# Performance work log

Measured on AMD Instinct MI355X. Metric: run time of the kernel, lower is better.

The kernel has to match this reference:

```python
import jax, jax.numpy as jnp
import numpy as np
import math

N = 8192
NFEAT = 63
NHID = 1024
NLAYERS = 7
LAMBDA = 1.5
ALPHA = 0.7
NEG = -1e12


def setup_inputs() -> dict:
    key = jax.random.key(0)
    ks = jax.random.split(key, 12)
    x = jax.random.normal(ks[0], (N, NFEAT), dtype=jnp.float32)
    # dist acts as a (normalized) propagation matrix; scale by 1/N for numerical stability
    dist = jax.random.uniform(ks[1], (N, N), dtype=jnp.float32) / N
    adj = jax.random.randint(ks[2], (N, N), 0, 2, dtype=jnp.int32)
    # parameters
    fc_W = jax.random.normal(ks[3], (NFEAT, NHID), dtype=jnp.float32) * 0.1
    fc_b = jnp.zeros((NHID,), dtype=jnp.float32)
    stdv = 1.0 / math.sqrt(NHID)
    conv_W = jax.random.uniform(ks[4], (NLAYERS, NHID, NHID), dtype=jnp.float32,
                                minval=-stdv, maxval=stdv)
    gat_W = jax.random.normal(ks[5], (NHID, NHID), dtype=jnp.float32) * (1.414 / math.sqrt(NHID))
    gat_a = jax.random.normal(ks[6], (2 * NHID, 1), dtype=jnp.float32) * 0.05
    cls1_W = jax.random.normal(ks[7], (NHID, 64), dtype=jnp.float32) * (1.0 / math.sqrt(NHID))
    cls1_b = jnp.zeros((64,), dtype=jnp.float32)
    cls3_W = jax.random.normal(ks[8], (64, 1), dtype=jnp.float32) * 0.125
    cls3_b = jnp.zeros((1,), dtype=jnp.float32)
    return {"x": x, "dist": dist, "adj": adj, "fc_W": fc_W, "fc_b": fc_b,
            "conv_W": conv_W, "gat_W": gat_W, "gat_a": gat_a,
            "cls1_W": cls1_W, "cls1_b": cls1_b, "cls3_W": cls3_W, "cls3_b": cls3_b}


def _theta(l):
    return min(1.0, math.log(LAMBDA / l + 1.0))


def reference(x, dist, adj, fc_W, fc_b, conv_W, gat_W, gat_a, cls1_W, cls1_b, cls3_W, cls3_b):
    # eval mode: all dropouts are identity
    h = jax.nn.relu(x @ fc_W + fc_b)          # [N, H]
    h0 = h
    # GCNII-style propagation layers
    for i in range(NLAYERS):
        theta = _theta(i + 1)
        hi = dist @ h                          # [N, H] sparse-style propagation
        support = (1.0 - ALPHA) * hi + ALPHA * h0
        out = theta * (support @ conv_W[i]) + (1.0 - theta) * support + h
        h = jax.nn.relu(out)
    # GAT layer (l = 9). Faithful math, but computed without the N*N*2F tensor:
    # e_ij = leakyrelu(h_i' @ a1 + h_j' @ a2) with h' = h @ W
    hp = h @ gat_W                             # [N, H]
    a1 = gat_a[:NHID, 0]                       # [H]
    a2 = gat_a[NHID:, 0]                       # [H]
    e = jax.nn.leaky_relu(hp @ a1[:, None] + (hp @ a2[:, None]).T, negative_slope=0.2)  # [N, N]
    e = jnp.where(adj > 0, e, NEG)
    attention = jax.nn.softmax(e, axis=1)      # [N, N]
    theta = _theta(9)
    hi = attention @ h                         # note: attends over layer input h, not hp
    support = (1.0 - ALPHA) * hi + ALPHA * h0
    out = theta * (support @ gat_W) + (1.0 - theta) * support + h
    h = jax.nn.elu(out)
    h = jax.nn.relu(h @ cls1_W + cls1_b)
    out = jax.nn.sigmoid(h @ cls3_W + cls3_b)  # [N, 1]
    return out.squeeze(-1)                     # [N]
```

## Files before the change

kernel.cpp:

```cpp
#include <hip/hip_runtime.h>
#include <math.h>

#define NN 8192
#define NH 1024

typedef __bf16 bf16x8 __attribute__((ext_vector_type(8)));
typedef float floatx4 __attribute__((ext_vector_type(4)));
typedef unsigned short us8 __attribute__((ext_vector_type(8)));
typedef unsigned short us;

__device__ __forceinline__ unsigned short f2bf(float f) {
  unsigned int u = __float_as_uint(f);
  u += 0x7fffu + ((u >> 16) & 1u);
  return (unsigned short)(u >> 16);
}

__device__ __forceinline__ void async16(const void* g, void* l) {
  __builtin_amdgcn_global_load_lds(
      (__attribute__((address_space(1))) void*)(g),
      (__attribute__((address_space(3))) void*)(l), 16, 0, 0);
}

__global__ __launch_bounds__(512)
void gemm_big(const us* __restrict__ A, const us* __restrict__ Bt,
              const float* __restrict__ aux, float* __restrict__ supf,
              us* __restrict__ supb)
{
  __shared__ __align__(16) us lsm[49152];
  us* lB = lsm;
  us* lA = lsm + 16384;

  const int id = blockIdx.x;
  const int yt = id & 31;
  const int xt = id >> 5;

  const int tid  = threadIdx.x;
  const int lane = tid & 63;
  const int wave = tid >> 6;
  const long tileM = (long)yt * 256;
  const long tileN = (long)xt * 128;
  const int wm = (wave & 3) * 64;
  const int wn = (wave >> 2) * 64;

  const int chunk = (tid & 3) ^ ((tid >> 3) & 3);
  const us* gAp = A + (tileM + (tid >> 2)) * 8192L + chunk * 8;
  const us* gBp = Bt + (tileN + (tid >> 2)) * 8192L + chunk * 8;
  const int lo = tid * 8;

  const int fr = lane & 15;
  const int q8 = (lane >> 4) * 8;
  const int q8x = q8 ^ ((fr & 6) << 2);

  floatx4 zero4 = {0.f, 0.f, 0.f, 0.f};
  floatx4 acc[4][4];
#pragma unroll
  for (int i = 0; i < 4; ++i)
#pragma unroll
    for (int j = 0; j < 4; ++j) acc[i][j] = zero4;

#define STAGE_BIG(s, kf)                                                  \
  {                                                                       \
    const long ko = (long)(kf) << 5;                                      \
    async16(gAp + ko, lA + (s)*8192 + lo);                                \
    async16(gAp + 128 * 8192L + ko, lA + (s)*8192 + 4096 + lo);           \
    async16(gBp + ko, lB + (s)*4096 + lo);                                \
  }

#define COMP_BIG(s)                                                      \
  {                                                                      \
    bf16x8 af[4], bfr[4];                                                \
    _Pragma("unroll") for (int i = 0; i < 4; ++i)                        \
        af[i] = *(const bf16x8*)&lA[(s)*8192 + (wm + 16 * i + fr) * 32 + q8x]; \
    _Pragma("unroll") for (int j = 0; j < 4; ++j)                        \
        bfr[j] = *(const bf16x8*)&lB[(s)*4096 + (wn + 16 * j + fr) * 32 + q8x]; \
    _Pragma("unroll") for (int i = 0; i < 4; ++i)                        \
        _Pragma("unroll") for (int j = 0; j < 4; ++j)                    \
            acc[i][j] = __builtin_amdgcn_mfma_f32_16x16x32_bf16(         \
                af[i], bfr[j], acc[i][j], 0, 0, 0);                      \
  }

#define WAITB asm volatile("s_waitcnt vmcnt(6)\n\ts_barrier" ::: "memory")

  STAGE_BIG(0, 0)
  STAGE_BIG(1, 1)
  STAGE_BIG(2, 2)

  for (int kt = 0; kt < 256; kt += 4) {
    int k3 = kt + 3; if (k3 > 255) k3 = 255;
    int k4 = kt + 4; if (k4 > 255) k4 = 255;
    int k5 = kt + 5; if (k5 > 255) k5 = 255;
    int k6 = kt + 6; if (k6 > 255) k6 = 255;
    WAITB; STAGE_BIG(3, k3) COMP_BIG(0)
    WAITB; STAGE_BIG(0, k4) COMP_BIG(1)
    WAITB; STAGE_BIG(1, k5) COMP_BIG(2)
    WAITB; STAGE_BIG(2, k6) COMP_BIG(3)
  }
  asm volatile("s_waitcnt vmcnt(0)" ::: "memory");

  const int crow = (lane >> 4) * 4;
#pragma unroll
  for (int i = 0; i < 4; ++i)
#pragma unroll
    for (int j = 0; j < 4; ++j)
#pragma unroll
      for (int r = 0; r < 4; ++r) {
        long row = tileM + wm + 16 * i + crow + r;
        long col = tileN + wn + 16 * j + fr;
        long idx = row * NH + col;
        float s = 0.3f * acc[i][j][r] + 0.7f * aux[idx];
        supf[idx] = s;
        supb[idx] = f2bf(s);
      }
#undef STAGE_BIG
#undef COMP_BIG
#undef WAITB
}

template<int EPI>
__global__ __launch_bounds__(256)
void gemm_db(const us* __restrict__ A, const us* __restrict__ Bt, int K,
             const float* __restrict__ aux, float* __restrict__ iof,
             us* __restrict__ outb, us* __restrict__ hTb, float theta)
{
  __shared__ __align__(16) us lsm[EPI == 1 ? 17408 : 16384];
  const int id = blockIdx.x;
  const int xcd = id & 7, slot = id >> 3;
  const int xt = slot & 7;
  const int yt = xcd + 8 * (slot >> 3);

  const int tid  = threadIdx.x;
  const int lane = tid & 63;
  const int wave = tid >> 6;
  const long tileM = (long)yt * 128;
  const long tileN = (long)xt * 128;
  const int wm = (wave & 1) * 64;
  const int wn = (wave >> 1) * 64;

  const int chunk = (tid & 3) ^ ((tid >> 3) & 3);
  const us* gA0 = A + (tileM + (tid >> 2)) * (long)K + chunk * 8;
  const us* gA1 = gA0 + 64L * K;
  const us* gB0 = Bt + (tileN + (tid >> 2)) * (long)K + chunk * 8;
  const us* gB1 = gB0 + 64L * K;
  us* lA = lsm;
  us* lB = lsm + 8192;
  const int lo = tid * 8;

  const int fr = lane & 15;
  const int q8 = (lane >> 4) * 8;
  const int q8x = q8 ^ ((fr & 6) << 2);

  floatx4 zero4 = {0.f, 0.f, 0.f, 0.f};
  floatx4 acc[4][4];
#pragma unroll
  for (int i = 0; i < 4; ++i)
#pragma unroll
    for (int j = 0; j < 4; ++j) acc[i][j] = zero4;

  async16(gA0, lA + lo);
  async16(gA1, lA + lo + 2048);
  async16(gB0, lB + lo);
  async16(gB1, lB + lo + 2048);

  const int nkt = K >> 5;
  for (int kt = 0; kt < nkt; ++kt) {
    const int b = (kt & 1) << 12;
    __syncthreads();
    if (kt + 1 < nkt) {
      const int k0 = (kt + 1) << 5;
      const int b2 = b ^ 4096;
      async16(gA0 + k0, lA + b2 + lo);
      async16(gA1 + k0, lA + b2 + lo + 2048);
      async16(gB0 + k0, lB + b2 + lo);
      async16(gB1 + k0, lB + b2 + lo + 2048);
    }
    bf16x8 af[4], bfr[4];
#pragma unroll
    for (int i = 0; i < 4; ++i)
      af[i] = *(const bf16x8*)&lA[b + (wm + 16 * i + fr) * 32 + q8x];
#pragma unroll
    for (int j = 0; j < 4; ++j)
      bfr[j] = *(const bf16x8*)&lB[b + (wn + 16 * j + fr) * 32 + q8x];
#pragma unroll
    for (int i = 0; i < 4; ++i)
#pragma unroll
      for (int j = 0; j < 4; ++j)
        acc[i][j] = __builtin_amdgcn_mfma_f32_16x16x32_bf16(af[i], bfr[j], acc[i][j], 0, 0, 0);
  }

  __syncthreads();
  us* ldsT = lsm;
  const int crow = (lane >> 4) * 4;
#pragma unroll
  for (int i = 0; i < 4; ++i) {
#pragma unroll
    for (int j = 0; j < 4; ++j) {
#pragma unroll
      for (int r = 0; r < 4; ++r) {
        int lr = wm + 16 * i + crow + r;
        int lc = wn + 16 * j + fr;
        long idx = (tileM + lr) * NH + tileN + lc;
        float o = theta * acc[i][j][r] + (1.f - theta) * aux[idx] + iof[idx];
        o = (EPI == 1) ? fmaxf(o, 0.f) : (o > 0.f ? o : __expf(o) - 1.f);
        iof[idx] = o;
        if (EPI == 1) ldsT[lc * 136 + lr] = f2bf(o);
        if (EPI == 2) outb[idx] = f2bf(o);
      }
    }
  }
  if (EPI == 1) {
    __syncthreads();
    int c = tid >> 1, half = tid & 1;
#pragma unroll
    for (int it = 0; it < 8; ++it) {
      int r = half * 64 + it * 8;
      us8 v = *(const us8*)&ldsT[c * 136 + r];
      *(us8*)&hTb[(tileN + c) * 8192L + tileM + r] = v;
    }
  }
}

__global__ __launch_bounds__(256)
void cls_gemm(const us* __restrict__ hb, const us* __restrict__ W1t,
              const float* __restrict__ b1, const float* __restrict__ W3,
              const float* __restrict__ b3, float* __restrict__ out)
{
  __shared__ __align__(16) us lA[4096];
  __shared__ __align__(16) us lB[2048];
  const int tid = threadIdx.x, lane = tid & 63, wave = tid >> 6;
  const long tileM = (long)blockIdx.x * 128;
  const us* gA0 = hb + (tileM + (tid >> 2)) * 1024L + (tid & 3) * 8;
  const us* gA1 = gA0 + 64 * 1024L;
  const us* gB0 = W1t + (tid >> 2) * 1024L + (tid & 3) * 8;
  const int fr = lane & 15, q8 = (lane >> 4) * 8;
  const int wm = wave * 32;

  floatx4 zero4 = {0.f, 0.f, 0.f, 0.f};
  floatx4 acc[2][4];
#pragma unroll
  for (int i = 0; i < 2; ++i)
#pragma unroll
    for (int j = 0; j < 4; ++j) acc[i][j] = zero4;

  for (int kt = 0; kt < 32; ++kt) {
    const int k0 = kt << 5;
    async16(gA0 + k0, lA + tid * 8);
    async16(gA1 + k0, lA + 2048 + tid * 8);
    async16(gB0 + k0, lB + tid * 8);
    __syncthreads();
    bf16x8 af[2], bfr[4];
#pragma unroll
    for (int i = 0; i < 2; ++i)
      af[i] = *(const bf16x8*)&lA[(wm + 16 * i + fr) * 32 + q8];
#pragma unroll
    for (int j = 0; j < 4; ++j)
      bfr[j] = *(const bf16x8*)&lB[(16 * j + fr) * 32 + q8];
#pragma unroll
    for (int i = 0; i < 2; ++i)
#pragma unroll
      for (int j = 0; j < 4; ++j)
        acc[i][j] = __builtin_amdgcn_mfma_f32_16x16x32_bf16(af[i], bfr[j], acc[i][j], 0, 0, 0);
    __syncthreads();
  }

  float b1v[4], w3v[4];
#pragma unroll
  for (int j = 0; j < 4; ++j) { b1v[j] = b1[16 * j + fr]; w3v[j] = W3[16 * j + fr]; }
  const float b3v = b3[0];
  const int crow = (lane >> 4) * 4;
#pragma unroll
  for (int i = 0; i < 2; ++i)
#pragma unroll
    for (int r = 0; r < 4; ++r) {
      float v = 0.f;
#pragma unroll
      for (int j = 0; j < 4; ++j)
        v += fmaxf(acc[i][j][r] + b1v[j], 0.f) * w3v[j];
      v += __shfl_xor(v, 1);
      v += __shfl_xor(v, 2);
      v += __shfl_xor(v, 4);
      v += __shfl_xor(v, 8);
      if (fr == 0)
        out[tileM + wm + 16 * i + crow + r] = 1.f / (1.f + __expf(-(v + b3v)));
    }
}

__global__ __launch_bounds__(256)
void transpose_f32_bf16(const float* __restrict__ src, us* __restrict__ dst,
                        int R, int C) {
  __shared__ float t[32][33];
  int tid = threadIdx.x;
  int tx = tid & 31, ty = tid >> 5;
  long r0 = (long)blockIdx.y * 32, c0 = (long)blockIdx.x * 32;
#pragma unroll
  for (int i = 0; i < 32; i += 8)
    t[ty + i][tx] = src[(r0 + ty + i) * C + c0 + tx];
  __syncthreads();
#pragma unroll
  for (int i = 0; i < 32; i += 8)
    dst[(c0 + ty + i) * R + r0 + tx] = f2bf(t[tx][ty + i]);
}

__global__ __launch_bounds__(256)
void f32_to_bf16_vec(const float* __restrict__ s, us* __restrict__ d) {
  long i = (blockIdx.x * 256L + threadIdx.x) * 4;
  float4 v = *(const float4*)(s + i);
  *(ushort4*)(d + i) = make_ushort4(f2bf(v.x), f2bf(v.y), f2bf(v.z), f2bf(v.w));
}

__global__ __launch_bounds__(256)
void fc_kernel(const float* __restrict__ x, const float* __restrict__ W,
               const float* __restrict__ b, float* __restrict__ h0f,
               float* __restrict__ hf) {
  __shared__ float xs[64];
  int row = blockIdx.x, tid = threadIdx.x;
  if (tid < 63) xs[tid] = x[row * 63 + tid];
  __syncthreads();
#pragma unroll
  for (int q = 0; q < 4; ++q) {
    int c = tid + q * 256;
    float s = b[c];
    for (int k = 0; k < 63; ++k) s += xs[k] * W[k * NH + c];
    s = fmaxf(s, 0.f);
    long idx = (long)row * NH + c;
    h0f[idx] = s;
    hf[idx] = s;
  }
}

__global__ __launch_bounds__(256)
void wv_kernel(const float* __restrict__ W, const float* __restrict__ a,
               float* __restrict__ va1, float* __restrict__ va2) {
  int k = blockIdx.x, tid = threadIdx.x;
  float s1 = 0.f, s2 = 0.f;
  for (int n = tid; n < NH; n += 256) {
    float w = W[(long)k * NH + n];
    s1 += w * a[n];
    s2 += w * a[NH + n];
  }
#pragma unroll
  for (int o = 32; o; o >>= 1) { s1 += __shfl_down(s1, o); s2 += __shfl_down(s2, o); }
  __shared__ float r1[4], r2[4];
  int wave = tid >> 6;
  if ((tid & 63) == 0) { r1[wave] = s1; r2[wave] = s2; }
  __syncthreads();
  if (tid == 0) {
    va1[k] = r1[0] + r1[1] + r1[2] + r1[3];
    va2[k] = r2[0] + r2[1] + r2[2] + r2[3];
  }
}

__global__ __launch_bounds__(256)
void fg_kernel(const float* __restrict__ h, const float* __restrict__ va1,
               const float* __restrict__ va2, float* __restrict__ fv,
               float* __restrict__ gv) {
  int row = blockIdx.x, tid = threadIdx.x;
  float s1 = 0.f, s2 = 0.f;
  for (int k = tid; k < NH; k += 256) {
    float v = h[(long)row * NH + k];
    s1 += v * va1[k];
    s2 += v * va2[k];
  }
#pragma unroll
  for (int o = 32; o; o >>= 1) { s1 += __shfl_down(s1, o); s2 += __shfl_down(s2, o); }
  __shared__ float r1[4], r2[4];
  int wave = tid >> 6;
  if ((tid & 63) == 0) { r1[wave] = s1; r2[wave] = s2; }
  __syncthreads();
  if (tid == 0) {
    fv[row] = r1[0] + r1[1] + r1[2] + r1[3];
    gv[row] = r2[0] + r2[1] + r2[2] + r2[3];
  }
}

__global__ __launch_bounds__(256)
void attn_ml(const int* __restrict__ adj, const float* __restrict__ f,
             const float* __restrict__ g, float* __restrict__ Mr,
             float* __restrict__ Lr) {
  const int row = blockIdx.x, tid = threadIdx.x;
  const float fi = f[row];
  const int4* arow = (const int4*)(adj + (long)row * NN);
  float m = -3.0e38f, s = 0.f;
  for (int c = tid; c < NN / 4; c += 256) {
    int4 a = arow[c];
    float4 gg = *(const float4*)(g + c * 4);
#pragma unroll
    for (int t = 0; t < 4; ++t) {
      int av = (t == 0) ? a.x : (t == 1) ? a.y : (t == 2) ? a.z : a.w;
      float gvv = (t == 0) ? gg.x : (t == 1) ? gg.y : (t == 2) ? gg.z : gg.w;
      if (av > 0) {
        float e = fi + gvv;
        e = e > 0.f ? e : 0.2f * e;
        if (e > m) { s = s * __expf(m - e) + 1.f; m = e; }
        else s += __expf(e - m);
      }
    }
  }
#pragma unroll
  for (int o = 32; o; o >>= 1) {
    float m2 = __shfl_down(m, o), s2 = __shfl_down(s, o);
    float mn = fmaxf(m, m2);
    s = s * __expf(m - mn) + s2 * __expf(m2 - mn);
    m = mn;
  }
  __shared__ float ms[4], ss[4];
  int wave = tid >> 6;
  if ((tid & 63) == 0) { ms[wave] = m; ss[wave] = s; }
  __syncthreads();
  if (tid == 0) {
    float mm = ms[0], sv = ss[0];
    for (int w = 1; w < 4; ++w) {
      float mn = fmaxf(mm, ms[w]);
      sv = sv * __expf(mm - mn) + ss[w] * __expf(ms[w] - mn);
      mm = mn;
    }
    Mr[row] = mm;
    Lr[row] = sv;
  }
}

__global__ __launch_bounds__(256)
void attn_p(const int* __restrict__ adj, const float* __restrict__ f,
            const float* __restrict__ g, const float* __restrict__ Mr,
            const float* __restrict__ Lr, us* __restrict__ P) {
  long gid = blockIdx.x * 256L + threadIdx.x;
  int row = (int)(gid >> 11);
  int jc = (int)(gid & 2047) * 4;
  float fi = f[row], m = Mr[row], l = Lr[row];
  bool uni = !(l > 0.f);
  float inv = uni ? 0.f : 1.f / l;
  int4 a = *(const int4*)(adj + ((long)row << 13) + jc);
  float4 gg = *(const float4*)(g + jc);
  float p[4];
#pragma unroll
  for (int t = 0; t < 4; ++t) {
    int av = (t == 0) ? a.x : (t == 1) ? a.y : (t == 2) ? a.z : a.w;
    float gvv = (t == 0) ? gg.x : (t == 1) ? gg.y : (t == 2) ? gg.z : gg.w;
    float e = fi + gvv;
    e = e > 0.f ? e : 0.2f * e;
    float pv = (av > 0) ? __expf(e - m) * inv : 0.f;
    if (uni) pv = 1.f / (float)NN;
    p[t] = pv;
  }
  *(ushort4*)(P + ((long)row << 13) + jc) =
      make_ushort4(f2bf(p[0]), f2bf(p[1]), f2bf(p[2]), f2bf(p[3]));
}

extern "C" void kernel_launch(void* const* d_in, const int* in_sizes, int n_in,
                              void* d_out, int out_size, void* d_ws, size_t ws_size,
                              hipStream_t stream) {
  const float* x      = (const float*)d_in[0];
  const float* dist   = (const float*)d_in[1];
  const int*   adj    = (const int*)d_in[2];
  const float* fc_W   = (const float*)d_in[3];
  const float* fc_b   = (const float*)d_in[4];
  const float* conv_W = (const float*)d_in[5];
  const float* gat_W  = (const float*)d_in[6];
  const float* gat_a  = (const float*)d_in[7];
  const float* cls1_W = (const float*)d_in[8];
  const float* cls1_b = (const float*)d_in[9];
  const float* cls3_W = (const float*)d_in[10];
  const float* cls3_b = (const float*)d_in[11];
  float* out = (float*)d_out;

  char* p = (char*)d_ws;
  auto alloc = [&](size_t bytes) {
    char* r = p;
    p += (bytes + 255) & ~(size_t)255;
    return r;
  };
  us* distb   = (us*)alloc((size_t)NN * NN * 2);
  float* h0f  = (float*)alloc((size_t)NN * NH * 4);
  float* hf   = (float*)alloc((size_t)NN * NH * 4);
  float* supf = (float*)alloc((size_t)NN * NH * 4);
  us* supb    = (us*)alloc((size_t)NN * NH * 2);
  us* hb      = (us*)alloc((size_t)NN * NH * 2);
  us* hTb     = (us*)alloc((size_t)NN * NH * 2);
  us* convWT  = (us*)alloc((size_t)7 * NH * NH * 2);
  us* gatWT   = (us*)alloc((size_t)NH * NH * 2);
  us* W1t     = (us*)alloc((size_t)64 * NH * 2);
  float* va1 = (float*)alloc(NH * 4);
  float* va2 = (float*)alloc(NH * 4);
  float* fv  = (float*)alloc(NN * 4);
  float* gv  = (float*)alloc(NN * 4);
  float* Mr  = (float*)alloc(NN * 4);
  float* Lr  = (float*)alloc(NN * 4);

  float th[7];
  for (int l = 0; l < 7; ++l) {
    float t = logf(1.5f / (float)(l + 1) + 1.f);
    th[l] = t < 1.f ? t : 1.f;
  }
  float th9 = logf(1.5f / 9.f + 1.f);

  f32_to_bf16_vec<<<(NN * (long)NN) / (4 * 256), 256, 0, stream>>>(dist, distb);
  for (int i = 0; i < 7; ++i)
    transpose_f32_bf16<<<dim3(32, 32), 256, 0, stream>>>(
        conv_W + (size_t)i * NH * NH, convWT + (size_t)i * NH * NH, NH, NH);
  transpose_f32_bf16<<<dim3(32, 32), 256, 0, stream>>>(gat_W, gatWT, NH, NH);
  transpose_f32_bf16<<<dim3(2, 32), 256, 0, stream>>>(cls1_W, W1t, NH, 64);

  fc_kernel<<<NN, 256, 0, stream>>>(x, fc_W, fc_b, h0f, hf);
  transpose_f32_bf16<<<dim3(NH / 32, NN / 32), 256, 0, stream>>>(hf, hTb, NN, NH);

  for (int l = 0; l < 7; ++l) {
    gemm_big<<<256, 512, 0, stream>>>(distb, hTb, h0f, supf, supb);
    gemm_db<1><<<512, 256, 0, stream>>>(supb, convWT + (size_t)l * NH * NH, NH,
                                        supf, hf, nullptr, hTb, th[l]);
  }

  wv_kernel<<<NH, 256, 0, stream>>>(gat_W, gat_a, va1, va2);
  fg_kernel<<<NN, 256, 0, stream>>>(hf, va1, va2, fv, gv);
  attn_ml<<<NN, 256, 0, stream>>>(adj, fv, gv, Mr, Lr);
  attn_p<<<(NN * (long)NN) / (4 * 256), 256, 0, stream>>>(adj, fv, gv, Mr, Lr, distb);

  gemm_big<<<256, 512, 0, stream>>>(distb, hTb, h0f, supf, supb);
  gemm_db<2><<<512, 256, 0, stream>>>(supb, gatWT, NH, supf, hf, hb, nullptr, th9);

  cls_gemm<<<64, 256, 0, stream>>>(hb, W1t, cls1_b, cls3_W, cls3_b, out);
}
```

Baseline: 2.378 ms.

## Restructure GEMM k-loops: load fragments before staging, 4-stage ring in gemm_db

In gemm_big, each k-step now reads its LDS fragments first, then issues the next async stage, then crosses a second barrier before running the MFMA block at raised wave priority behind sched_barriers. gemm_db moves from a double-buffered loop with per-iteration __syncthreads to the same 4-stage async ring with vmcnt-based waits, using a fixed 32 k-tiles (K=1024) and more shared memory. The aim is to hide global-to-LDS latency and keep the matrix units busy. In exchange it adds an extra barrier per step, raises LDS use (lower occupancy), and hardcodes K to 1024 in gemm_db.

```diff
diff --git a/kernel.cpp b/kernel.cpp
--- a/kernel.cpp
+++ b/kernel.cpp
@@ -66,20 +66,27 @@
     async16(gBp + ko, lB + (s)*4096 + lo);                                \
   }
 
-#define COMP_BIG(s)                                                      \
-  {                                                                      \
-    bf16x8 af[4], bfr[4];                                                \
-    _Pragma("unroll") for (int i = 0; i < 4; ++i)                        \
+#define KSTEP_BIG(s, kf)                                                  \
+  {                                                                       \
+    asm volatile("s_waitcnt vmcnt(6)" ::: "memory");                      \
+    __builtin_amdgcn_s_barrier();                                         \
+    bf16x8 af[4], bfr[4];                                                 \
+    _Pragma("unroll") for (int i = 0; i < 4; ++i)                         \
         af[i] = *(const bf16x8*)&lA[(s)*8192 + (wm + 16 * i + fr) * 32 + q8x]; \
-    _Pragma("unroll") for (int j = 0; j < 4; ++j)                        \
+    _Pragma("unroll") for (int j = 0; j < 4; ++j)                         \
         bfr[j] = *(const bf16x8*)&lB[(s)*4096 + (wn + 16 * j + fr) * 32 + q8x]; \
-    _Pragma("unroll") for (int i = 0; i < 4; ++i)                        \
-        _Pragma("unroll") for (int j = 0; j < 4; ++j)                    \
-            acc[i][j] = __builtin_amdgcn_mfma_f32_16x16x32_bf16(         \
-                af[i], bfr[j], acc[i][j], 0, 0, 0);                      \
-  }
-
-#define WAITB asm volatile("s_waitcnt vmcnt(6)\n\ts_barrier" ::: "memory")
+    STAGE_BIG((((s) + 3) & 3), kf);                                       \
+    __builtin_amdgcn_s_barrier();                                         \
+    asm volatile("s_waitcnt lgkmcnt(0)" ::: "memory");                    \
+    __builtin_amdgcn_sched_barrier(0);                                    \
+    __builtin_amdgcn_s_setprio(1);                                        \
+    _Pragma("unroll") for (int i = 0; i < 4; ++i)                         \
+        _Pragma("unroll") for (int j = 0; j < 4; ++j)                     \
+            acc[i][j] = __builtin_amdgcn_mfma_f32_16x16x32_bf16(          \
+                af[i], bfr[j], acc[i][j], 0, 0, 0);                       \
+    __builtin_amdgcn_s_setprio(0);                                        \
+    __builtin_amdgcn_sched_barrier(0);                                    \
+  }
 
   STAGE_BIG(0, 0)
   STAGE_BIG(1, 1)
@@ -90,10 +97,10 @@
     int k4 = kt + 4; if (k4 > 255) k4 = 255;
     int k5 = kt + 5; if (k5 > 255) k5 = 255;
     int k6 = kt + 6; if (k6 > 255) k6 = 255;
-    WAITB; STAGE_BIG(3, k3) COMP_BIG(0)
-    WAITB; STAGE_BIG(0, k4) COMP_BIG(1)
-    WAITB; STAGE_BIG(1, k5) COMP_BIG(2)
-    WAITB; STAGE_BIG(2, k6) COMP_BIG(3)
+    KSTEP_BIG(0, k3)
+    KSTEP_BIG(1, k4)
+    KSTEP_BIG(2, k5)
+    KSTEP_BIG(3, k6)
   }
   asm volatile("s_waitcnt vmcnt(0)" ::: "memory");
 
@@ -112,8 +119,7 @@
         supb[idx] = f2bf(s);
       }
 #undef STAGE_BIG
-#undef COMP_BIG
-#undef WAITB
+#undef KSTEP_BIG
 }
 
 template<int EPI>
@@ -122,7 +128,10 @@
              const float* __restrict__ aux, float* __restrict__ iof,
              us* __restrict__ outb, us* __restrict__ hTb, float theta)
 {
-  __shared__ __align__(16) us lsm[EPI == 1 ? 17408 : 16384];
+  __shared__ __align__(16) us lsm[32768];
+  us* lB = lsm;
+  us* lA = lsm + 16384;
+
   const int id = blockIdx.x;
   const int xcd = id & 7, slot = id >> 3;
   const int xt = slot & 7;
@@ -141,8 +150,6 @@
   const us* gA1 = gA0 + 64L * K;
   const us* gB0 = Bt + (tileN + (tid >> 2)) * (long)K + chunk * 8;
   const us* gB1 = gB0 + 64L * K;
-  us* lA = lsm;
-  us* lB = lsm + 8192;
   const int lo = tid * 8;
 
   const int fr = lane & 15;
@@ -156,38 +163,54 @@
 #pragma unroll
     for (int j = 0; j < 4; ++j) acc[i][j] = zero4;
 
-  async16(gA0, lA + lo);
-  async16(gA1, lA + lo + 2048);
-  async16(gB0, lB + lo);
-  async16(gB1, lB + lo + 2048);
-
-  const int nkt = K >> 5;
-  for (int kt = 0; kt < nkt; ++kt) {
-    const int b = (kt & 1) << 12;
-    __syncthreads();
-    if (kt + 1 < nkt) {
-      const int k0 = (kt + 1) << 5;
-      const int b2 = b ^ 4096;
-      async16(gA0 + k0, lA + b2 + lo);
-      async16(gA1 + k0, lA + b2 + lo + 2048);
-      async16(gB0 + k0, lB + b2 + lo);
-      async16(gB1 + k0, lB + b2 + lo + 2048);
-    }
-    bf16x8 af[4], bfr[4];
-#pragma unroll
-    for (int i = 0; i < 4; ++i)
-      af[i] = *(const bf16x8*)&lA[b + (wm + 16 * i + fr) * 32 + q8x];
-#pragma unroll
-    for (int j = 0; j < 4; ++j)
-      bfr[j] = *(const bf16x8*)&lB[b + (wn + 16 * j + fr) * 32 + q8x];
-#pragma unroll
-    for (int i = 0; i < 4; ++i)
-#pragma unroll
-      for (int j = 0; j < 4; ++j)
-        acc[i][j] = __builtin_amdgcn_mfma_f32_16x16x32_bf16(af[i], bfr[j], acc[i][j], 0, 0, 0);
-  }
-
+#define STAGE_DB(s, kf)                                                   \
+  {                                                                       \
+    const int k0 = (kf) << 5;                                             \
+    async16(gA0 + k0, lA + (s)*4096 + lo);                                \
+    async16(gA1 + k0, lA + (s)*4096 + 2048 + lo);                         \
+    async16(gB0 + k0, lB + (s)*4096 + lo);                                \
+    async16(gB1 + k0, lB + (s)*4096 + 2048 + lo);                         \
+  }
+
+#define KSTEP_DB(s, kf)                                                   \
+  {                                                                       \
+    asm volatile("s_waitcnt vmcnt(8)" ::: "memory");                      \
+    __builtin_amdgcn_s_barrier();                                         \
+    bf16x8 af[4], bfr[4];                                                 \
+    _Pragma("unroll") for (int i = 0; i < 4; ++i)                         \
+        af[i] = *(const bf16x8*)&lA[(s)*4096 + (wm + 16 * i + fr) * 32 + q8x]; \
+    _Pragma("unroll") for (int j = 0; j < 4; ++j)                         \
+        bfr[j] = *(const bf16x8*)&lB[(s)*4096 + (wn + 16 * j + fr) * 32 + q8x]; \
+    STAGE_DB((((s) + 3) & 3), kf);                                        \
+    __builtin_amdgcn_s_barrier();                                         \
+    asm volatile("s_waitcnt lgkmcnt(0)" ::: "memory");                    \
+    __builtin_amdgcn_sched_barrier(0);                                    \
+    __builtin_amdgcn_s_setprio(1);                                        \
+    _Pragma("unroll") for (int i = 0; i < 4; ++i)                         \
+        _Pragma("unroll") for (int j = 0; j < 4; ++j)                     \
+            acc[i][j] = __builtin_amdgcn_mfma_f32_16x16x32_bf16(          \
+                af[i], bfr[j], acc[i][j], 0, 0, 0);                       \
+    __builtin_amdgcn_s_setprio(0);                                        \
+    __builtin_amdgcn_sched_barrier(0);                                    \
+  }
+
+  STAGE_DB(0, 0)
+  STAGE_DB(1, 1)
+  STAGE_DB(2, 2)
+
+  for (int kt = 0; kt < 32; kt += 4) {
+    int k3 = kt + 3; if (k3 > 31) k3 = 31;
+    int k4 = kt + 4; if (k4 > 31) k4 = 31;
+    int k5 = kt + 5; if (k5 > 31) k5 = 31;
+    int k6 = kt + 6; if (k6 > 31) k6 = 31;
+    KSTEP_DB(0, k3)
+    KSTEP_DB(1, k4)
+    KSTEP_DB(2, k5)
+    KSTEP_DB(3, k6)
+  }
+  asm volatile("s_waitcnt vmcnt(0)" ::: "memory");
   __syncthreads();
+
   us* ldsT = lsm;
   const int crow = (lane >> 4) * 4;
 #pragma unroll
@@ -217,6 +240,8 @@
       *(us8*)&hTb[(tileN + c) * 8192L + tileM + r] = v;
     }
   }
+#undef STAGE_DB
+#undef KSTEP_DB
 }
 
 __global__ __launch_bounds__(256)
```

Result: slower. 2.449 ms (+3.0%).
